# Performance work log

Hardware: AMD Instinct MI355X
Metric: run time of the kernel (lower is better)

The kernel has to match this reference:

```python
import jax, jax.numpy as jnp
import numpy as np
import math

B, N, D, H = 2, 96, 64, 4  # batch, num_nodes, d_model, num_heads
DK = D // H


def setup_inputs() -> dict:
    key = jax.random.key(0)
    ks = jax.random.split(key, 11)
    s = 0.02
    return {
        "state": jax.random.normal(ks[0], (B, N * N, D), jnp.float32),
        "w_lk": jax.random.normal(ks[1], (D, D), jnp.float32) * s,
        "b_lk": jax.random.normal(ks[2], (D,), jnp.float32) * s,
        "w_rk": jax.random.normal(ks[3], (D, D), jnp.float32) * s,
        "b_rk": jax.random.normal(ks[4], (D,), jnp.float32) * s,
        "w_lv": jax.random.normal(ks[5], (D, D), jnp.float32) * s,
        "b_lv": jax.random.normal(ks[6], (D,), jnp.float32) * s,
        "w_rv": jax.random.normal(ks[7], (D, D), jnp.float32) * s,
        "b_rv": jax.random.normal(ks[8], (D,), jnp.float32) * s,
        "w_out": jax.random.normal(ks[9], (D, D), jnp.float32) * s,
        "b_out": jax.random.normal(ks[10], (D,), jnp.float32) * s,
    }


def reference(state, w_lk, b_lk, w_rk, b_rk, w_lv, b_lv, w_rv, b_rv, w_out, b_out):
    b = state.shape[0]
    n = int(np.sqrt(state.shape[1]))
    d_model = state.shape[2]
    h, dk = H, d_model // H

    def lin(x, w, bias):  # torch nn.Linear: x @ W^T + b
        return x @ w.T + bias

    # project and view as [b, n, n, h, dk]
    lk = lin(state, w_lk, b_lk).reshape(b, n, n, h, dk)
    rk = lin(state, w_rk, b_rk).reshape(b, n, n, h, dk)
    lv = lin(state, w_lv, b_lv).reshape(b, n, n, h, dk)
    rv = lin(state, w_rv, b_rv).reshape(b, n, n, h, dk)

    # triangular edge-attention scores over intermediate node a
    scores = jnp.einsum('bxahd,bayhd->bxayh', lk, rk) / math.sqrt(dk)
    att = jax.nn.softmax(scores, axis=2)  # softmax over a

    # fused contraction: equivalent to val = lv[x,a]*rv[a,y] then sum_a att*val,
    # without materializing the O(n^3 * d) val tensor
    x = jnp.einsum('bxayh,bxahd,bayhd->bxyhd', att, lv, rv)

    x = x.reshape(b, n * n, d_model)
    return lin(x, w_out, b_out)
```

## Files before the change

kernel.cpp:

```cpp
#include <hip/hip_runtime.h>

#define TENS   1179648
#define HM     147456
#define T_ROWS 18432
#define NP_S   6

__global__ __launch_bounds__(256) void proj4_kernel(
    const float* __restrict__ state,
    const float* __restrict__ w0, const float* __restrict__ b0,
    const float* __restrict__ w1, const float* __restrict__ b1,
    const float* __restrict__ w2, const float* __restrict__ b2,
    const float* __restrict__ w3, const float* __restrict__ b3,
    float* __restrict__ o0, float* __restrict__ o1,
    float* __restrict__ o2, float* __restrict__ o3)
{
    __shared__ float swt[64 * 68];
    __shared__ float srow[64 * 68];
    __shared__ float sb[64];
    const int t = threadIdx.x;
    const int row0 = blockIdx.x * 64;

#pragma unroll
    for (int j = 0; j < 4; ++j) {
        const int s = t + j * 256;
        const int row = s >> 4, k4 = s & 15;
        *(float4*)&srow[row * 68 + k4 * 4] =
            *(const float4*)(state + (size_t)(row0 + row) * 64 + k4 * 4);
    }
    const int b   = row0 / 9216;
    const int rb0 = row0 - b * 9216;
    const int c4 = t & 15, rg = t >> 4;
    const int h  = c4 >> 2;
    const int dq = c4 & 3;

    for (int mat = 0; mat < 4; ++mat) {
        const float* w  = (mat == 0) ? w0 : (mat == 1) ? w1 : (mat == 2) ? w2 : w3;
        const float* bi = (mat == 0) ? b0 : (mat == 1) ? b1 : (mat == 2) ? b2 : b3;
        float* o        = (mat == 0) ? o0 : (mat == 1) ? o1 : (mat == 2) ? o2 : o3;

        __syncthreads();
#pragma unroll
        for (int j = 0; j < 4; ++j) {
            const int s = t + j * 256;
            const int c = s >> 4, k4 = s & 15;
            const float4 wv = *(const float4*)(w + c * 64 + k4 * 4);
            swt[(k4 * 4 + 0) * 68 + c] = wv.x;
            swt[(k4 * 4 + 1) * 68 + c] = wv.y;
            swt[(k4 * 4 + 2) * 68 + c] = wv.z;
            swt[(k4 * 4 + 3) * 68 + c] = wv.w;
        }
        if (t < 64) sb[t] = bi[t];
        __syncthreads();

        const float4 binit = *(const float4*)&sb[c4 * 4];
        float4 acc[4];
#pragma unroll
        for (int rr = 0; rr < 4; ++rr) acc[rr] = binit;
#pragma unroll
        for (int k4 = 0; k4 < 16; ++k4) {
            const float4 wq0 = *(const float4*)&swt[(k4 * 4 + 0) * 68 + c4 * 4];
            const float4 wq1 = *(const float4*)&swt[(k4 * 4 + 1) * 68 + c4 * 4];
            const float4 wq2 = *(const float4*)&swt[(k4 * 4 + 2) * 68 + c4 * 4];
            const float4 wq3 = *(const float4*)&swt[(k4 * 4 + 3) * 68 + c4 * 4];
#pragma unroll
            for (int rr = 0; rr < 4; ++rr) {
                const float4 s4 = *(const float4*)&srow[(rg + rr * 16) * 68 + k4 * 4];
                acc[rr].x = fmaf(s4.x, wq0.x, acc[rr].x);
                acc[rr].y = fmaf(s4.x, wq0.y, acc[rr].y);
                acc[rr].z = fmaf(s4.x, wq0.z, acc[rr].z);
                acc[rr].w = fmaf(s4.x, wq0.w, acc[rr].w);
                acc[rr].x = fmaf(s4.y, wq1.x, acc[rr].x);
                acc[rr].y = fmaf(s4.y, wq1.y, acc[rr].y);
                acc[rr].z = fmaf(s4.y, wq1.z, acc[rr].z);
                acc[rr].w = fmaf(s4.y, wq1.w, acc[rr].w);
                acc[rr].x = fmaf(s4.z, wq2.x, acc[rr].x);
                acc[rr].y = fmaf(s4.z, wq2.y, acc[rr].y);
                acc[rr].z = fmaf(s4.z, wq2.z, acc[rr].z);
                acc[rr].w = fmaf(s4.z, wq2.w, acc[rr].w);
                acc[rr].x = fmaf(s4.w, wq3.x, acc[rr].x);
                acc[rr].y = fmaf(s4.w, wq3.y, acc[rr].y);
                acc[rr].z = fmaf(s4.w, wq3.z, acc[rr].z);
                acc[rr].w = fmaf(s4.w, wq3.w, acc[rr].w);
            }
        }
        float* dp = o + (size_t)(b * 4 + h) * HM + dq * 4;
#pragma unroll
        for (int rr = 0; rr < 4; ++rr)
            *(float4*)(dp + (size_t)(rb0 + rg + rr * 16) * 16) = acc[rr];
    }
}

__global__ __launch_bounds__(256) void fused_attn_kernel(
    const float* __restrict__ lk, const float* __restrict__ rk,
    const float* __restrict__ lv, const float* __restrict__ rv,
    float* __restrict__ nump, float* __restrict__ denp)
{
    __shared__ float lk_s[2176];
    __shared__ float lv_s[2176];
    __shared__ float rk_s[2560];
    __shared__ float rv_s[2560];

    const int t = threadIdx.x;
    const int j = blockIdx.x;
    const int bh = j & 7;
    const int r2 = j >> 3;
    const int sc = r2 % 6;
    const int tile = r2 / 6;
    const int xt = tile % 3, yt = tile / 3;
    const int x0 = xt * 32, y0 = yt * 32;
    const int a00 = sc * 16;
    const int xi2 = t & 15, yi2 = t >> 4;

    const float* plk = lk + (size_t)bh * HM;
    const float* prk = rk + (size_t)bh * HM;
    const float* plv = lv + (size_t)bh * HM;
    const float* prv = rv + (size_t)bh * HM;

    const int slot1 = t + 256;
    const int xl0 = t >> 4,     lrem0 = t & 15,     lai0 = lrem0 >> 2, lc0 = lrem0 & 3;
    const int xl1 = slot1 >> 4, lrem1 = slot1 & 15, lai1 = lrem1 >> 2, lc1 = lrem1 & 3;
    const int ar0 = t >> 7,     rrem0 = t & 127,    yl0 = rrem0 >> 2,  rc0 = rrem0 & 3;
    const int ar1 = slot1 >> 7, rrem1 = slot1 & 127, yl1 = rrem1 >> 2, rc1 = rrem1 & 3;

    const float* glk0 = plk + ((x0 + xl0) * 96 + a00 + lai0) * 16 + lc0 * 4;
    const float* glk1 = plk + ((x0 + xl1) * 96 + a00 + lai1) * 16 + lc1 * 4;
    const float* glv0 = plv + ((x0 + xl0) * 96 + a00 + lai0) * 16 + lc0 * 4;
    const float* glv1 = plv + ((x0 + xl1) * 96 + a00 + lai1) * 16 + lc1 * 4;
    const float* grk0 = prk + ((a00 + ar0) * 96 + y0 + yl0) * 16 + rc0 * 4;
    const float* grk1 = prk + ((a00 + ar1) * 96 + y0 + yl1) * 16 + rc1 * 4;
    const float* grv0 = prv + ((a00 + ar0) * 96 + y0 + yl0) * 16 + rc0 * 4;
    const float* grv1 = prv + ((a00 + ar1) * 96 + y0 + yl1) * 16 + rc1 * 4;

    const int llo0 = ((xl0 & 1) * 16 + (xl0 >> 1)) * 68 + lai0 * 16 + lc0 * 4;
    const int llo1 = ((xl1 & 1) * 16 + (xl1 >> 1)) * 68 + lai1 * 16 + lc1 * 4;
    const int rlo0 = ar0 * 640 + ((yl0 & 1) * 16 + (yl0 >> 1)) * 20 + rc0 * 4;
    const int rlo1 = ar1 * 640 + ((yl1 & 1) * 16 + (yl1 >> 1)) * 20 + rc1 * 4;

    float4 p_lk0 = *(const float4*)glk0, p_lk1 = *(const float4*)glk1;
    float4 p_lv0 = *(const float4*)glv0, p_lv1 = *(const float4*)glv1;
    float4 p_rk0 = *(const float4*)grk0, p_rk1 = *(const float4*)grk1;
    float4 p_rv0 = *(const float4*)grv0, p_rv1 = *(const float4*)grv1;

    float4 a00v = {0.f,0.f,0.f,0.f}, a01v = a00v, a02v = a00v, a03v = a00v;
    float4 a10v = a00v, a11v = a00v, a12v = a00v, a13v = a00v;
    float4 a20v = a00v, a21v = a00v, a22v = a00v, a23v = a00v;
    float4 a30v = a00v, a31v = a00v, a32v = a00v, a33v = a00v;
    float d00 = 0.f, d01 = 0.f, d10 = 0.f, d11 = 0.f;

    for (int acx = 0; acx < 4; ++acx) {
        __syncthreads();
        *(float4*)&lk_s[llo0] = p_lk0;  *(float4*)&lk_s[llo1] = p_lk1;
        *(float4*)&lv_s[llo0] = p_lv0;  *(float4*)&lv_s[llo1] = p_lv1;
        *(float4*)&rk_s[rlo0] = p_rk0;  *(float4*)&rk_s[rlo1] = p_rk1;
        *(float4*)&rv_s[rlo0] = p_rv0;  *(float4*)&rv_s[rlo1] = p_rv1;
        __syncthreads();
        if (acx < 3) {
            glk0 += 64;   glk1 += 64;   glv0 += 64;   glv1 += 64;
            grk0 += 6144; grk1 += 6144; grv0 += 6144; grv1 += 6144;
            p_lk0 = *(const float4*)glk0; p_lk1 = *(const float4*)glk1;
            p_lv0 = *(const float4*)glv0; p_lv1 = *(const float4*)glv1;
            p_rk0 = *(const float4*)grk0; p_rk1 = *(const float4*)grk1;
            p_rv0 = *(const float4*)grv0; p_rv1 = *(const float4*)grv1;
        }
#pragma unroll
        for (int ai = 0; ai < 4; ++ai) {
            const int lo0 = xi2 * 68 + ai * 16;
            const int lo1 = (16 + xi2) * 68 + ai * 16;
            const int ro0 = ai * 640 + yi2 * 20;
            const int ro1 = ai * 640 + (16 + yi2) * 20;
            const float4 ka0 = *(const float4*)&lk_s[lo0];
            const float4 ka1 = *(const float4*)&lk_s[lo0 + 4];
            const float4 ka2 = *(const float4*)&lk_s[lo0 + 8];
            const float4 ka3 = *(const float4*)&lk_s[lo0 + 12];
            const float4 kb0 = *(const float4*)&lk_s[lo1];
            const float4 kb1 = *(const float4*)&lk_s[lo1 + 4];
            const float4 kb2 = *(const float4*)&lk_s[lo1 + 8];
            const float4 kb3 = *(const float4*)&lk_s[lo1 + 12];
            const float4 qa0 = *(const float4*)&rk_s[ro0];
            const float4 qa1 = *(const float4*)&rk_s[ro0 + 4];
            const float4 qa2 = *(const float4*)&rk_s[ro0 + 8];
            const float4 qa3 = *(const float4*)&rk_s[ro0 + 12];
            const float4 qb0 = *(const float4*)&rk_s[ro1];
            const float4 qb1 = *(const float4*)&rk_s[ro1 + 4];
            const float4 qb2 = *(const float4*)&rk_s[ro1 + 8];
            const float4 qb3 = *(const float4*)&rk_s[ro1 + 12];

#define DOT16(A0,A1,A2,A3,B0,B1,B2,B3)                                   \
    fmaf(A3.w,B3.w, fmaf(A3.z,B3.z, fmaf(A3.y,B3.y, fmaf(A3.x,B3.x,     \
    fmaf(A2.w,B2.w, fmaf(A2.z,B2.z, fmaf(A2.y,B2.y, fmaf(A2.x,B2.x,     \
    fmaf(A1.w,B1.w, fmaf(A1.z,B1.z, fmaf(A1.y,B1.y, fmaf(A1.x,B1.x,     \
    fmaf(A0.w,B0.w, fmaf(A0.z,B0.z, fmaf(A0.y,B0.y, A0.x*B0.x)))))))))))))))
            const float s00 = DOT16(ka0,ka1,ka2,ka3, qa0,qa1,qa2,qa3);
            const float s01 = DOT16(ka0,ka1,ka2,ka3, qb0,qb1,qb2,qb3);
            const float s10 = DOT16(kb0,kb1,kb2,kb3, qa0,qa1,qa2,qa3);
            const float s11 = DOT16(kb0,kb1,kb2,kb3, qb0,qb1,qb2,qb3);
#undef DOT16
            const float p00 = __expf(s00 * 0.25f);
            const float p01 = __expf(s01 * 0.25f);
            const float p10 = __expf(s10 * 0.25f);
            const float p11 = __expf(s11 * 0.25f);
            d00 += p00; d01 += p01; d10 += p10; d11 += p11;

            const float4 la0 = *(const float4*)&lv_s[lo0];
            const float4 la1 = *(const float4*)&lv_s[lo0 + 4];
            const float4 la2 = *(const float4*)&lv_s[lo0 + 8];
            const float4 la3 = *(const float4*)&lv_s[lo0 + 12];
            const float4 lb0 = *(const float4*)&lv_s[lo1];
            const float4 lb1 = *(const float4*)&lv_s[lo1 + 4];
            const float4 lb2 = *(const float4*)&lv_s[lo1 + 8];
            const float4 lb3 = *(const float4*)&lv_s[lo1 + 12];
            const float4 va0 = *(const float4*)&rv_s[ro0];
            const float4 va1 = *(const float4*)&rv_s[ro0 + 4];
            const float4 va2 = *(const float4*)&rv_s[ro0 + 8];
            const float4 va3 = *(const float4*)&rv_s[ro0 + 12];
            const float4 vb0 = *(const float4*)&rv_s[ro1];
            const float4 vb1 = *(const float4*)&rv_s[ro1 + 4];
            const float4 vb2 = *(const float4*)&rv_s[ro1 + 8];
            const float4 vb3 = *(const float4*)&rv_s[ro1 + 12];

#define ACC4(AC, P, L, V)                       \
    AC.x = fmaf(P * L.x, V.x, AC.x);            \
    AC.y = fmaf(P * L.y, V.y, AC.y);            \
    AC.z = fmaf(P * L.z, V.z, AC.z);            \
    AC.w = fmaf(P * L.w, V.w, AC.w);
            ACC4(a00v, p00, la0, va0) ACC4(a01v, p00, la1, va1)
            ACC4(a02v, p00, la2, va2) ACC4(a03v, p00, la3, va3)
            ACC4(a10v, p01, la0, vb0) ACC4(a11v, p01, la1, vb1)
            ACC4(a12v, p01, la2, vb2) ACC4(a13v, p01, la3, vb3)
            ACC4(a20v, p10, lb0, va0) ACC4(a21v, p10, lb1, va1)
            ACC4(a22v, p10, lb2, va2) ACC4(a23v, p10, lb3, va3)
            ACC4(a30v, p11, lb0, vb0) ACC4(a31v, p11, lb1, vb1)
            ACC4(a32v, p11, lb2, vb2) ACC4(a33v, p11, lb3, vb3)
#undef ACC4
        }
    }

    const size_t pb = (size_t)(sc * 8 + bh) * 9216;
    const int xA = x0 + 2 * xi2, yA = y0 + 2 * yi2;
    {
        const size_t rb = pb + (size_t)xA * 96 + yA;
        float4* np = (float4*)(nump + rb * 16);
        np[0] = a00v; np[1] = a01v; np[2] = a02v; np[3] = a03v;
        denp[rb] = d00;
    }
    {
        const size_t rb = pb + (size_t)xA * 96 + yA + 1;
        float4* np = (float4*)(nump + rb * 16);
        np[0] = a10v; np[1] = a11v; np[2] = a12v; np[3] = a13v;
        denp[rb] = d01;
    }
    {
        const size_t rb = pb + (size_t)(xA + 1) * 96 + yA;
        float4* np = (float4*)(nump + rb * 16);
        np[0] = a20v; np[1] = a21v; np[2] = a22v; np[3] = a23v;
        denp[rb] = d10;
    }
    {
        const size_t rb = pb + (size_t)(xA + 1) * 96 + yA + 1;
        float4* np = (float4*)(nump + rb * 16);
        np[0] = a30v; np[1] = a31v; np[2] = a32v; np[3] = a33v;
        denp[rb] = d11;
    }
}

__global__ __launch_bounds__(256) void proj1_kernel(
    const float* __restrict__ nump, const float* __restrict__ denp,
    const float* __restrict__ w, const float* __restrict__ bi,
    float* __restrict__ out)
{
    __shared__ float swt[64 * 68];
    __shared__ float srow[64 * 68];
    __shared__ float sb[64];
    const int t = threadIdx.x;
    const int row0 = blockIdx.x * 64;
    const int bb  = row0 / 9216;
    const int rb0 = row0 - bb * 9216;

#pragma unroll
    for (int j = 0; j < 4; ++j) {
        const int s = t + j * 256;
        const int c = s >> 4, k4 = s & 15;
        const float4 wv = *(const float4*)(w + c * 64 + k4 * 4);
        swt[(k4 * 4 + 0) * 68 + c] = wv.x;
        swt[(k4 * 4 + 1) * 68 + c] = wv.y;
        swt[(k4 * 4 + 2) * 68 + c] = wv.z;
        swt[(k4 * 4 + 3) * 68 + c] = wv.w;
    }
#pragma unroll
    for (int j = 0; j < 4; ++j) {
        const int s = t + j * 256;
        const int rl = s >> 4, hc = s & 15;
        const int bh = bb * 4 + (hc >> 2);
        const int c4g = hc & 3;
        const int rb = rb0 + rl;
        float sx = 0.f, sy = 0.f, sz = 0.f, sw4 = 0.f, dd = 0.f;
#pragma unroll
        for (int sc = 0; sc < NP_S; ++sc) {
            const size_t rbs = (size_t)(sc * 8 + bh) * 9216 + rb;
            const float4 v = *(const float4*)(nump + rbs * 16 + c4g * 4);
            sx += v.x; sy += v.y; sz += v.z; sw4 += v.w;
            dd += denp[rbs];
        }
        const float inv = 1.0f / dd;
        float4 ov; ov.x = sx * inv; ov.y = sy * inv; ov.z = sz * inv; ov.w = sw4 * inv;
        *(float4*)&srow[rl * 68 + hc * 4] = ov;
    }
    if (t < 64) sb[t] = bi[t];
    __syncthreads();

    const int c4 = t & 15, rg = t >> 4;
    const float4 binit = *(const float4*)&sb[c4 * 4];
    float4 acc[4];
#pragma unroll
    for (int rr = 0; rr < 4; ++rr) acc[rr] = binit;
#pragma unroll
    for (int k4 = 0; k4 < 16; ++k4) {
        const float4 wq0 = *(const float4*)&swt[(k4 * 4 + 0) * 68 + c4 * 4];
        const float4 wq1 = *(const float4*)&swt[(k4 * 4 + 1) * 68 + c4 * 4];
        const float4 wq2 = *(const float4*)&swt[(k4 * 4 + 2) * 68 + c4 * 4];
        const float4 wq3 = *(const float4*)&swt[(k4 * 4 + 3) * 68 + c4 * 4];
#pragma unroll
        for (int rr = 0; rr < 4; ++rr) {
            const float4 s4 = *(const float4*)&srow[(rg + rr * 16) * 68 + k4 * 4];
            acc[rr].x = fmaf(s4.x, wq0.x, acc[rr].x);
            acc[rr].y = fmaf(s4.x, wq0.y, acc[rr].y);
            acc[rr].z = fmaf(s4.x, wq0.z, acc[rr].z);
            acc[rr].w = fmaf(s4.x, wq0.w, acc[rr].w);
            acc[rr].x = fmaf(s4.y, wq1.x, acc[rr].x);
            acc[rr].y = fmaf(s4.y, wq1.y, acc[rr].y);
            acc[rr].z = fmaf(s4.y, wq1.z, acc[rr].z);
            acc[rr].w = fmaf(s4.y, wq1.w, acc[rr].w);
            acc[rr].x = fmaf(s4.z, wq2.x, acc[rr].x);
            acc[rr].y = fmaf(s4.z, wq2.y, acc[rr].y);
            acc[rr].z = fmaf(s4.z, wq2.z, acc[rr].z);
            acc[rr].w = fmaf(s4.z, wq2.w, acc[rr].w);
            acc[rr].x = fmaf(s4.w, wq3.x, acc[rr].x);
            acc[rr].y = fmaf(s4.w, wq3.y, acc[rr].y);
            acc[rr].z = fmaf(s4.w, wq3.z, acc[rr].z);
            acc[rr].w = fmaf(s4.w, wq3.w, acc[rr].w);
        }
    }
#pragma unroll
    for (int rr = 0; rr < 4; ++rr)
        *(float4*)(out + (size_t)(row0 + rg + rr * 16) * 64 + c4 * 4) = acc[rr];
}

extern "C" void kernel_launch(void* const* d_in, const int* in_sizes, int n_in,
                              void* d_out, int out_size, void* d_ws, size_t ws_size,
                              hipStream_t stream)
{
    const float* state = (const float*)d_in[0];
    const float* w_lk  = (const float*)d_in[1];
    const float* b_lk  = (const float*)d_in[2];
    const float* w_rk  = (const float*)d_in[3];
    const float* b_rk  = (const float*)d_in[4];
    const float* w_lv  = (const float*)d_in[5];
    const float* b_lv  = (const float*)d_in[6];
    const float* w_rv  = (const float*)d_in[7];
    const float* b_rv  = (const float*)d_in[8];
    const float* w_out = (const float*)d_in[9];
    const float* b_out = (const float*)d_in[10];
    float* out = (float*)d_out;

    float* ws = (float*)d_ws;
    float* lk   = ws;
    float* rk   = ws + (size_t)TENS;
    float* lv   = ws + (size_t)2 * TENS;
    float* rv   = ws + (size_t)3 * TENS;
    float* nump = ws + (size_t)4 * TENS;
    float* denp = nump + (size_t)NP_S * 8 * 9216 * 16;

    proj4_kernel<<<T_ROWS / 64, 256, 0, stream>>>(
        state, w_lk, b_lk, w_rk, b_rk, w_lv, b_lv, w_rv, b_rv, lk, rk, lv, rv);
    fused_attn_kernel<<<432, 256, 0, stream>>>(lk, rk, lv, rv, nump, denp);
    proj1_kernel<<<T_ROWS / 64, 256, 0, stream>>>(nump, denp, w_out, b_out, out);
}
```

Baseline: 124.6 us.

## Retile edge attention to 48x24 tiles with 3x3 outputs per thread

New measurement: 139.2 us. +11.7%, slower.

```diff
diff --git a/kernel.cpp b/kernel.cpp
--- a/kernel.cpp
+++ b/kernel.cpp
@@ -4,6 +4,12 @@
 #define HM     147456
 #define T_ROWS 18432
 #define NP_S   6
+
+#define DOT16(A0,A1,A2,A3,B0,B1,B2,B3)                                   \
+    fmaf(A3.w,B3.w, fmaf(A3.z,B3.z, fmaf(A3.y,B3.y, fmaf(A3.x,B3.x,     \
+    fmaf(A2.w,B2.w, fmaf(A2.z,B2.z, fmaf(A2.y,B2.y, fmaf(A2.x,B2.x,     \
+    fmaf(A1.w,B1.w, fmaf(A1.z,B1.z, fmaf(A1.y,B1.y, fmaf(A1.x,B1.x,     \
+    fmaf(A0.w,B0.w, fmaf(A0.z,B0.z, fmaf(A0.y,B0.y, A0.x*B0.x)))))))))))))))
 
 __global__ __launch_bounds__(256) void proj4_kernel(
     const float* __restrict__ state,
@@ -90,15 +96,15 @@
     }
 }
 
-__global__ __launch_bounds__(256) void fused_attn_kernel(
+__global__ __launch_bounds__(128, 1) void fused_attn_kernel(
     const float* __restrict__ lk, const float* __restrict__ rk,
     const float* __restrict__ lv, const float* __restrict__ rv,
     float* __restrict__ nump, float* __restrict__ denp)
 {
-    __shared__ float lk_s[2176];
-    __shared__ float lv_s[2176];
-    __shared__ float rk_s[2560];
-    __shared__ float rv_s[2560];
+    __shared__ float lk_s[48 * 68];
+    __shared__ float lv_s[48 * 68];
+    __shared__ float rk_s[4 * 24 * 20];
+    __shared__ float rv_s[4 * 24 * 20];
 
     const int t = threadIdx.x;
     const int j = blockIdx.x;
@@ -106,160 +112,130 @@
     const int r2 = j >> 3;
     const int sc = r2 % 6;
     const int tile = r2 / 6;
-    const int xt = tile % 3, yt = tile / 3;
-    const int x0 = xt * 32, y0 = yt * 32;
-    const int a00 = sc * 16;
-    const int xi2 = t & 15, yi2 = t >> 4;
+    const int xt = tile & 1, yt = tile >> 1;
+    const int x0 = xt * 48, y0 = yt * 24;
+    const int a0 = sc * 16;
+    const int xi = t & 15, yi = t >> 4;
 
     const float* plk = lk + (size_t)bh * HM;
     const float* prk = rk + (size_t)bh * HM;
     const float* plv = lv + (size_t)bh * HM;
     const float* prv = rv + (size_t)bh * HM;
 
-    const int slot1 = t + 256;
-    const int xl0 = t >> 4,     lrem0 = t & 15,     lai0 = lrem0 >> 2, lc0 = lrem0 & 3;
-    const int xl1 = slot1 >> 4, lrem1 = slot1 & 15, lai1 = lrem1 >> 2, lc1 = lrem1 & 3;
-    const int ar0 = t >> 7,     rrem0 = t & 127,    yl0 = rrem0 >> 2,  rc0 = rrem0 & 3;
-    const int ar1 = slot1 >> 7, rrem1 = slot1 & 127, yl1 = rrem1 >> 2, rc1 = rrem1 & 3;
-
-    const float* glk0 = plk + ((x0 + xl0) * 96 + a00 + lai0) * 16 + lc0 * 4;
-    const float* glk1 = plk + ((x0 + xl1) * 96 + a00 + lai1) * 16 + lc1 * 4;
-    const float* glv0 = plv + ((x0 + xl0) * 96 + a00 + lai0) * 16 + lc0 * 4;
-    const float* glv1 = plv + ((x0 + xl1) * 96 + a00 + lai1) * 16 + lc1 * 4;
-    const float* grk0 = prk + ((a00 + ar0) * 96 + y0 + yl0) * 16 + rc0 * 4;
-    const float* grk1 = prk + ((a00 + ar1) * 96 + y0 + yl1) * 16 + rc1 * 4;
-    const float* grv0 = prv + ((a00 + ar0) * 96 + y0 + yl0) * 16 + rc0 * 4;
-    const float* grv1 = prv + ((a00 + ar1) * 96 + y0 + yl1) * 16 + rc1 * 4;
-
-    const int llo0 = ((xl0 & 1) * 16 + (xl0 >> 1)) * 68 + lai0 * 16 + lc0 * 4;
-    const int llo1 = ((xl1 & 1) * 16 + (xl1 >> 1)) * 68 + lai1 * 16 + lc1 * 4;
-    const int rlo0 = ar0 * 640 + ((yl0 & 1) * 16 + (yl0 >> 1)) * 20 + rc0 * 4;
-    const int rlo1 = ar1 * 640 + ((yl1 & 1) * 16 + (yl1 >> 1)) * 20 + rc1 * 4;
-
-    float4 p_lk0 = *(const float4*)glk0, p_lk1 = *(const float4*)glk1;
-    float4 p_lv0 = *(const float4*)glv0, p_lv1 = *(const float4*)glv1;
-    float4 p_rk0 = *(const float4*)grk0, p_rk1 = *(const float4*)grk1;
-    float4 p_rv0 = *(const float4*)grv0, p_rv1 = *(const float4*)grv1;
-
-    float4 a00v = {0.f,0.f,0.f,0.f}, a01v = a00v, a02v = a00v, a03v = a00v;
-    float4 a10v = a00v, a11v = a00v, a12v = a00v, a13v = a00v;
-    float4 a20v = a00v, a21v = a00v, a22v = a00v, a23v = a00v;
-    float4 a30v = a00v, a31v = a00v, a32v = a00v, a33v = a00v;
-    float d00 = 0.f, d01 = 0.f, d10 = 0.f, d11 = 0.f;
+    float4 acc[3][3][4];
+    float  den[3][3];
+#pragma unroll
+    for (int i = 0; i < 3; ++i)
+#pragma unroll
+        for (int jc = 0; jc < 3; ++jc) {
+            den[i][jc] = 0.f;
+#pragma unroll
+            for (int q = 0; q < 4; ++q)
+                acc[i][jc][q] = make_float4(0.f, 0.f, 0.f, 0.f);
+        }
 
     for (int acx = 0; acx < 4; ++acx) {
+        const int abase = a0 + acx * 4;
         __syncthreads();
-        *(float4*)&lk_s[llo0] = p_lk0;  *(float4*)&lk_s[llo1] = p_lk1;
-        *(float4*)&lv_s[llo0] = p_lv0;  *(float4*)&lv_s[llo1] = p_lv1;
-        *(float4*)&rk_s[rlo0] = p_rk0;  *(float4*)&rk_s[rlo1] = p_rk1;
-        *(float4*)&rv_s[rlo0] = p_rv0;  *(float4*)&rv_s[rlo1] = p_rv1;
+#pragma unroll
+        for (int jj = 0; jj < 6; ++jj) {
+            const int s = t + jj * 128;
+            const int xl = s >> 4, rem = s & 15, ai = rem >> 2, c = rem & 3;
+            const size_t g = ((size_t)(x0 + xl) * 96 + abase + ai) * 16 + c * 4;
+            const int lo = xl * 68 + ai * 16 + c * 4;
+            *(float4*)&lk_s[lo] = *(const float4*)(plk + g);
+            *(float4*)&lv_s[lo] = *(const float4*)(plv + g);
+        }
+#pragma unroll
+        for (int jj = 0; jj < 4; ++jj) {
+            const int s = t + jj * 128;
+            const int ai = s >> 7, rem = s & 127, yl = rem >> 2, c = rem & 3;
+            if (yl < 24) {
+                const size_t g = ((size_t)(abase + ai) * 96 + y0 + yl) * 16 + c * 4;
+                const int ro = ai * 480 + yl * 20 + c * 4;
+                *(float4*)&rk_s[ro] = *(const float4*)(prk + g);
+                *(float4*)&rv_s[ro] = *(const float4*)(prv + g);
+            }
+        }
         __syncthreads();
-        if (acx < 3) {
-            glk0 += 64;   glk1 += 64;   glv0 += 64;   glv1 += 64;
-            grk0 += 6144; grk1 += 6144; grv0 += 6144; grv1 += 6144;
-            p_lk0 = *(const float4*)glk0; p_lk1 = *(const float4*)glk1;
-            p_lv0 = *(const float4*)glv0; p_lv1 = *(const float4*)glv1;
-            p_rk0 = *(const float4*)grk0; p_rk1 = *(const float4*)grk1;
-            p_rv0 = *(const float4*)grv0; p_rv1 = *(const float4*)grv1;
-        }
-#pragma unroll
-        for (int ai = 0; ai < 4; ++ai) {
-            const int lo0 = xi2 * 68 + ai * 16;
-            const int lo1 = (16 + xi2) * 68 + ai * 16;
-            const int ro0 = ai * 640 + yi2 * 20;
-            const int ro1 = ai * 640 + (16 + yi2) * 20;
-            const float4 ka0 = *(const float4*)&lk_s[lo0];
-            const float4 ka1 = *(const float4*)&lk_s[lo0 + 4];
-            const float4 ka2 = *(const float4*)&lk_s[lo0 + 8];
-            const float4 ka3 = *(const float4*)&lk_s[lo0 + 12];
-            const float4 kb0 = *(const float4*)&lk_s[lo1];
-            const float4 kb1 = *(const float4*)&lk_s[lo1 + 4];
-            const float4 kb2 = *(const float4*)&lk_s[lo1 + 8];
-            const float4 kb3 = *(const float4*)&lk_s[lo1 + 12];
-            const float4 qa0 = *(const float4*)&rk_s[ro0];
-            const float4 qa1 = *(const float4*)&rk_s[ro0 + 4];
-            const float4 qa2 = *(const float4*)&rk_s[ro0 + 8];
-            const float4 qa3 = *(const float4*)&rk_s[ro0 + 12];
-            const float4 qb0 = *(const float4*)&rk_s[ro1];
-            const float4 qb1 = *(const float4*)&rk_s[ro1 + 4];
-            const float4 qb2 = *(const float4*)&rk_s[ro1 + 8];
-            const float4 qb3 = *(const float4*)&rk_s[ro1 + 12];
-
-#define DOT16(A0,A1,A2,A3,B0,B1,B2,B3)                                   \
-    fmaf(A3.w,B3.w, fmaf(A3.z,B3.z, fmaf(A3.y,B3.y, fmaf(A3.x,B3.x,     \
-    fmaf(A2.w,B2.w, fmaf(A2.z,B2.z, fmaf(A2.y,B2.y, fmaf(A2.x,B2.x,     \
-    fmaf(A1.w,B1.w, fmaf(A1.z,B1.z, fmaf(A1.y,B1.y, fmaf(A1.x,B1.x,     \
-    fmaf(A0.w,B0.w, fmaf(A0.z,B0.z, fmaf(A0.y,B0.y, A0.x*B0.x)))))))))))))))
-            const float s00 = DOT16(ka0,ka1,ka2,ka3, qa0,qa1,qa2,qa3);
-            const float s01 = DOT16(ka0,ka1,ka2,ka3, qb0,qb1,qb2,qb3);
-            const float s10 = DOT16(kb0,kb1,kb2,kb3, qa0,qa1,qa2,qa3);
-            const float s11 = DOT16(kb0,kb1,kb2,kb3, qb0,qb1,qb2,qb3);
-#undef DOT16
-            const float p00 = __expf(s00 * 0.25f);
-            const float p01 = __expf(s01 * 0.25f);
-            const float p10 = __expf(s10 * 0.25f);
-            const float p11 = __expf(s11 * 0.25f);
-            d00 += p00; d01 += p01; d10 += p10; d11 += p11;
-
-            const float4 la0 = *(const float4*)&lv_s[lo0];
-            const float4 la1 = *(const float4*)&lv_s[lo0 + 4];
-            const float4 la2 = *(const float4*)&lv_s[lo0 + 8];
-            const float4 la3 = *(const float4*)&lv_s[lo0 + 12];
-            const float4 lb0 = *(const float4*)&lv_s[lo1];
-            const float4 lb1 = *(const float4*)&lv_s[lo1 + 4];
-            const float4 lb2 = *(const float4*)&lv_s[lo1 + 8];
-            const float4 lb3 = *(const float4*)&lv_s[lo1 + 12];
-            const float4 va0 = *(const float4*)&rv_s[ro0];
-            const float4 va1 = *(const float4*)&rv_s[ro0 + 4];
-            const float4 va2 = *(const float4*)&rv_s[ro0 + 8];
-            const float4 va3 = *(const float4*)&rv_s[ro0 + 12];
-            const float4 vb0 = *(const float4*)&rv_s[ro1];
-            const float4 vb1 = *(const float4*)&rv_s[ro1 + 4];
-            const float4 vb2 = *(const float4*)&rv_s[ro1 + 8];
-            const float4 vb3 = *(const float4*)&rv_s[ro1 + 12];
-
-#define ACC4(AC, P, L, V)                       \
-    AC.x = fmaf(P * L.x, V.x, AC.x);            \
-    AC.y = fmaf(P * L.y, V.y, AC.y);            \
-    AC.z = fmaf(P * L.z, V.z, AC.z);            \
-    AC.w = fmaf(P * L.w, V.w, AC.w);
-            ACC4(a00v, p00, la0, va0) ACC4(a01v, p00, la1, va1)
-            ACC4(a02v, p00, la2, va2) ACC4(a03v, p00, la3, va3)
-            ACC4(a10v, p01, la0, vb0) ACC4(a11v, p01, la1, vb1)
-            ACC4(a12v, p01, la2, vb2) ACC4(a13v, p01, la3, vb3)
-            ACC4(a20v, p10, lb0, va0) ACC4(a21v, p10, lb1, va1)
-            ACC4(a22v, p10, lb2, va2) ACC4(a23v, p10, lb3, va3)
-            ACC4(a30v, p11, lb0, vb0) ACC4(a31v, p11, lb1, vb1)
-            ACC4(a32v, p11, lb2, vb2) ACC4(a33v, p11, lb3, vb3)
-#undef ACC4
+
+#pragma unroll
+        for (int asel = 0; asel < 4; ++asel) {
+            float4 ka[3][4];
+#pragma unroll
+            for (int i = 0; i < 3; ++i) {
+                const int lo = (xi + 16 * i) * 68 + asel * 16;
+#pragma unroll
+                for (int q = 0; q < 4; ++q)
+                    ka[i][q] = *(const float4*)&lk_s[lo + q * 4];
+            }
+            float p[3][3];
+#pragma unroll
+            for (int jc = 0; jc < 3; ++jc) {
+                const int ro = asel * 480 + (yi + 8 * jc) * 20;
+                const float4 q0 = *(const float4*)&rk_s[ro];
+                const float4 q1 = *(const float4*)&rk_s[ro + 4];
+                const float4 q2 = *(const float4*)&rk_s[ro + 8];
+                const float4 q3 = *(const float4*)&rk_s[ro + 12];
+#pragma unroll
+                for (int i = 0; i < 3; ++i) {
+                    const float sv = DOT16(ka[i][0], ka[i][1], ka[i][2], ka[i][3],
+                                           q0, q1, q2, q3);
+                    const float pv = __expf(sv * 0.25f);
+                    p[i][jc] = pv;
+                    den[i][jc] += pv;
+                }
+            }
+            float4 la[3][4];
+#pragma unroll
+            for (int i = 0; i < 3; ++i) {
+                const int lo = (xi + 16 * i) * 68 + asel * 16;
+#pragma unroll
+                for (int q = 0; q < 4; ++q)
+                    la[i][q] = *(const float4*)&lv_s[lo + q * 4];
+            }
+#pragma unroll
+            for (int jc = 0; jc < 3; ++jc) {
+                const int ro = asel * 480 + (yi + 8 * jc) * 20;
+                const float4 v0 = *(const float4*)&rv_s[ro];
+                const float4 v1 = *(const float4*)&rv_s[ro + 4];
+                const float4 v2 = *(const float4*)&rv_s[ro + 8];
+                const float4 v3 = *(const float4*)&rv_s[ro + 12];
+#pragma unroll
+                for (int i = 0; i < 3; ++i) {
+                    const float pp = p[i][jc];
+                    acc[i][jc][0].x = fmaf(pp * la[i][0].x, v0.x, acc[i][jc][0].x);
+                    acc[i][jc][0].y = fmaf(pp * la[i][0].y, v0.y, acc[i][jc][0].y);
+                    acc[i][jc][0].z = fmaf(pp * la[i][0].z, v0.z, acc[i][jc][0].z);
+                    acc[i][jc][0].w = fmaf(pp * la[i][0].w, v0.w, acc[i][jc][0].w);
+                    acc[i][jc][1].x = fmaf(pp * la[i][1].x, v1.x, acc[i][jc][1].x);
+                    acc[i][jc][1].y = fmaf(pp * la[i][1].y, v1.y, acc[i][jc][1].y);
+                    acc[i][jc][1].z = fmaf(pp * la[i][1].z, v1.z, acc[i][jc][1].z);
+                    acc[i][jc][1].w = fmaf(pp * la[i][1].w, v1.w, acc[i][jc][1].w);
+                    acc[i][jc][2].x = fmaf(pp * la[i][2].x, v2.x, acc[i][jc][2].x);
+                    acc[i][jc][2].y = fmaf(pp * la[i][2].y, v2.y, acc[i][jc][2].y);
+                    acc[i][jc][2].z = fmaf(pp * la[i][2].z, v2.z, acc[i][jc][2].z);
+                    acc[i][jc][2].w = fmaf(pp * la[i][2].w, v2.w, acc[i][jc][2].w);
+                    acc[i][jc][3].x = fmaf(pp * la[i][3].x, v3.x, acc[i][jc][3].x);
+                    acc[i][jc][3].y = fmaf(pp * la[i][3].y, v3.y, acc[i][jc][3].y);
+                    acc[i][jc][3].z = fmaf(pp * la[i][3].z, v3.z, acc[i][jc][3].z);
+                    acc[i][jc][3].w = fmaf(pp * la[i][3].w, v3.w, acc[i][jc][3].w);
+                }
+            }
         }
     }
 
     const size_t pb = (size_t)(sc * 8 + bh) * 9216;
-    const int xA = x0 + 2 * xi2, yA = y0 + 2 * yi2;
-    {
-        const size_t rb = pb + (size_t)xA * 96 + yA;
-        float4* np = (float4*)(nump + rb * 16);
-        np[0] = a00v; np[1] = a01v; np[2] = a02v; np[3] = a03v;
-        denp[rb] = d00;
-    }
-    {
-        const size_t rb = pb + (size_t)xA * 96 + yA + 1;
-        float4* np = (float4*)(nump + rb * 16);
-        np[0] = a10v; np[1] = a11v; np[2] = a12v; np[3] = a13v;
-        denp[rb] = d01;
-    }
-    {
-        const size_t rb = pb + (size_t)(xA + 1) * 96 + yA;
-        float4* np = (float4*)(nump + rb * 16);
-        np[0] = a20v; np[1] = a21v; np[2] = a22v; np[3] = a23v;
-        denp[rb] = d10;
-    }
-    {
-        const size_t rb = pb + (size_t)(xA + 1) * 96 + yA + 1;
-        float4* np = (float4*)(nump + rb * 16);
-        np[0] = a30v; np[1] = a31v; np[2] = a32v; np[3] = a33v;
-        denp[rb] = d11;
+#pragma unroll
+    for (int i = 0; i < 3; ++i) {
+#pragma unroll
+        for (int jc = 0; jc < 3; ++jc) {
+            const size_t rb = pb + (size_t)(x0 + xi + 16 * i) * 96 + (y0 + yi + 8 * jc);
+            float4* np = (float4*)(nump + rb * 16);
+            np[0] = acc[i][jc][0]; np[1] = acc[i][jc][1];
+            np[2] = acc[i][jc][2]; np[3] = acc[i][jc][3];
+            denp[rb] = den[i][jc];
+        }
     }
 }
 
@@ -372,6 +348,6 @@
 
     proj4_kernel<<<T_ROWS / 64, 256, 0, stream>>>(
         state, w_lk, b_lk, w_rk, b_rk, w_lv, b_lv, w_rv, b_rv, lk, rk, lv, rv);
-    fused_attn_kernel<<<432, 256, 0, stream>>>(lk, rk, lv, rv, nump, denp);
+    fused_attn_kernel<<<384, 128, 0, stream>>>(lk, rk, lv, rv, nump, denp);
     proj1_kernel<<<T_ROWS / 64, 256, 0, stream>>>(nump, denp, w_out, b_out, out);
 }
```
